# Kernel optimization log

Hardware: AMD Instinct MI355X
Metric: run time of the kernel (lower is better)

## Reference

```python
import jax, jax.numpy as jnp
import numpy as np

BN_EPS = 1e-5


def setup_inputs() -> dict:
    key = jax.random.key(0)
    ks = jax.random.split(key, 8)
    N, Cin, Cout, D, H, W = 4, 512, 256, 256, 128, 128
    feat_ffm = jax.random.normal(ks[0], (N, Cin, H, W), dtype=jnp.float32)
    coarse_x = jax.random.normal(ks[1], (N, D, H, W), dtype=jnp.float32)
    # conv1: 1x1, no bias; BN (eval mode: running stats); conv2: 1x1 with bias
    w1 = jax.random.normal(ks[2], (Cout, Cin), dtype=jnp.float32) * (1.0 / np.sqrt(Cin))
    bn_gamma = jnp.ones((Cout,), dtype=jnp.float32)
    bn_beta = jnp.zeros((Cout,), dtype=jnp.float32)
    bn_mean = jax.random.normal(ks[3], (Cout,), dtype=jnp.float32) * 0.1
    bn_var = jax.random.uniform(ks[4], (Cout,), dtype=jnp.float32, minval=0.5, maxval=1.5)
    w2 = jax.random.normal(ks[5], (Cout, Cout), dtype=jnp.float32) * (1.0 / np.sqrt(Cout))
    b2 = jnp.zeros((Cout,), dtype=jnp.float32)
    return {"feat_ffm": feat_ffm, "coarse_x": coarse_x, "w1": w1,
            "bn_gamma": bn_gamma, "bn_beta": bn_beta, "bn_mean": bn_mean,
            "bn_var": bn_var, "w2": w2, "b2": b2}


def reference(feat_ffm, coarse_x, w1, bn_gamma, bn_beta, bn_mean, bn_var, w2, b2):
    N, D, H, W = coarse_x.shape
    # conv1 (1x1) + BN(eval) + ReLU; Dropout2d is identity in eval mode
    x = jnp.einsum('nihw,oi->nohw', feat_ffm, w1)
    scale = bn_gamma * jax.lax.rsqrt(bn_var + BN_EPS)
    x = x * scale[None, :, None, None] + (bn_beta - bn_mean * scale)[None, :, None, None]
    x = jax.nn.relu(x)  # [N, C, H, W]
    C = x.shape[1]
    q = coarse_x.reshape(N, D, H * W)          # proj_query / proj_value
    k = x.reshape(N, C, H * W)                 # proj_key (pre-permute)
    energy = jnp.einsum('nds,ncs->ndc', q, k)  # [N, D, C]
    energy_new = jnp.max(energy, axis=-1, keepdims=True) - energy
    attention = jax.nn.softmax(energy_new, axis=-1)        # [N, D, C]
    out = jnp.einsum('ndc,nds->ncs', attention, q)         # attention^T @ value
    out = out.reshape(N, C, H, W)
    out = jnp.einsum('nchw,oc->nohw', out, w2) + b2[None, :, None, None]
    return out
```

## Files before the change

kernel.cpp:

```cpp
#include <hip/hip_runtime.h>


#define S_DIM 16384
#define C_DIM 256
#define CIN 512

typedef unsigned short u16;
typedef __attribute__((ext_vector_type(8))) short bf16x8;
typedef __attribute__((ext_vector_type(4))) float f32x4;

__device__ __forceinline__ u16 f2bf(float x) {
    unsigned u = __float_as_uint(x);
    u += 0x7fff + ((u >> 16) & 1);
    return (u16)(u >> 16);
}
__device__ __forceinline__ float bf2f(u16 h) {
    return __uint_as_float(((unsigned)h) << 16);
}
__device__ __forceinline__ void gld16(const u16* g, u16* l) {
    __builtin_amdgcn_global_load_lds((const __attribute__((address_space(1))) void*)g,
                                     (__attribute__((address_space(3))) void*)l, 16, 0, 0);
}
__device__ __forceinline__ void gld16f(const float* g, float* l) {
    __builtin_amdgcn_global_load_lds((const __attribute__((address_space(1))) void*)g,
                                     (__attribute__((address_space(3))) void*)l, 16, 0, 0);
}

__global__ __launch_bounds__(256) void prep_kernel(
    const float* __restrict__ coarse, const float* __restrict__ w1,
    const float* __restrict__ gamma, const float* __restrict__ beta,
    const float* __restrict__ mean, const float* __restrict__ var,
    u16* __restrict__ qhi, u16* __restrict__ qlo,
    u16* __restrict__ w1hi, u16* __restrict__ w1lo, float* __restrict__ b1) {
    int b = blockIdx.x;
    int t = threadIdx.x;
    if (b < 4096) {
        size_t i = (size_t)b * 256 + t;
        for (size_t c = i; c < 4194304u; c += 1048576u) {
            float4 v = ((const float4*)coarse)[c];
            float vv[4] = {v.x, v.y, v.z, v.w};
            u16 h[4], l[4];
#pragma unroll
            for (int j = 0; j < 4; ++j) {
                h[j] = f2bf(vv[j]);
                l[j] = f2bf(vv[j] - bf2f(h[j]));
            }
            *(uint2*)&qhi[c * 4] = *(uint2*)h;
            *(uint2*)&qlo[c * 4] = *(uint2*)l;
        }
    } else {
        int o = (b - 4096) * 16 + (t >> 4);
        int lane16 = t & 15;
        float sc = gamma[o] * rsqrtf(var[o] + 1e-5f);
        for (int i = lane16; i < CIN; i += 16) {
            float v = w1[o * CIN + i] * sc;
            u16 h = f2bf(v);
            w1hi[o * CIN + i] = h;
            w1lo[o * CIN + i] = f2bf(v - bf2f(h));
        }
        if (lane16 == 0) b1[o] = beta[o] - mean[o] * sc;
    }
}

__global__ __launch_bounds__(256) void conv_kernel(
    const u16* __restrict__ w1hi, const u16* __restrict__ w1lo,
    const float* __restrict__ feat, const float* __restrict__ b1,
    u16* __restrict__ khi, u16* __restrict__ klo) {
    __shared__ u16 AhS[4096], AlS[4096];
    __shared__ float BfS[4096];
    int s0 = blockIdx.x * 128;
    int m0 = blockIdx.y * 128;
    int bz = blockIdx.z;
    int tid = threadIdx.x, wave = tid >> 6, lane = tid & 63;
    int quad = lane >> 4, l15 = lane & 15;
    int wm = wave >> 1, wn = wave & 1;

    const u16* gAh0 = w1hi + (size_t)(m0 + lane) * CIN + wave * 8;
    const u16* gAh1 = w1hi + (size_t)(m0 + 64 + lane) * CIN + wave * 8;
    const u16* gAl0 = w1lo + (size_t)(m0 + lane) * CIN + wave * 8;
    const u16* gAl1 = w1lo + (size_t)(m0 + 64 + lane) * CIN + wave * 8;
    u16* dAh = AhS + wave * 1024;
    u16* dAl = AlS + wave * 1024;
    int bcol = ((lane & 31) * 4) ^ ((wave & 1) << 4);
    const float* gB = feat + (size_t)bz * ((size_t)CIN * S_DIM)
                    + (size_t)(8 * wave + (lane >> 5)) * S_DIM + s0 + bcol;
    float* dB = BfS + wave * 1024;

    f32x4 zero = {0.f, 0.f, 0.f, 0.f};
    f32x4 acc[4][4];
#pragma unroll
    for (int i = 0; i < 4; ++i)
#pragma unroll
        for (int j = 0; j < 4; ++j) acc[i][j] = zero;

    for (int kb = 0; kb < CIN; kb += 32) {
        __syncthreads();
        gld16(gAh0 + kb, dAh);
        gld16(gAh1 + kb, dAh + 512);
        gld16(gAl0 + kb, dAl);
        gld16(gAl1 + kb, dAl + 512);
#pragma unroll
        for (int p = 0; p < 4; ++p)
            gld16f(gB + (size_t)(kb + 2 * p) * S_DIM, dB + p * 256);
        __syncthreads();

        bf16x8 a_h[4], a_l[4];
        int aOff = quad * 1024 + (wm * 64 + l15) * 8;
#pragma unroll
        for (int t = 0; t < 4; ++t) {
            a_h[t] = *(const bf16x8*)&AhS[aOff + t * 128];
            a_l[t] = *(const bf16x8*)&AlS[aOff + t * 128];
        }
        bf16x8 b_h[4], b_l[4];
        int fl = (quad & 1) << 4;
        const float* Brow = BfS + quad * 1024;
#pragma unroll
        for (int nt = 0; nt < 4; ++nt) {
            int nf = (wn * 64 + nt * 16 + l15) ^ fl;
            union { unsigned d[4]; bf16x8 v; } H, L;
#pragma unroll
            for (int d = 0; d < 4; ++d) {
                float fa = Brow[(2 * d) * 128 + nf];
                float fb = Brow[(2 * d + 1) * 128 + nf];
                unsigned ua = __float_as_uint(fa), ub = __float_as_uint(fb);
                unsigned ra = ua + 0x7fffu + ((ua >> 16) & 1);
                unsigned rb = ub + 0x7fffu + ((ub >> 16) & 1);
                H.d[d] = __byte_perm(ra, rb, 0x7632);
                unsigned la = __float_as_uint(fa - __uint_as_float(ra & 0xffff0000u));
                unsigned lb = __float_as_uint(fb - __uint_as_float(rb & 0xffff0000u));
                la += 0x7fffu + ((la >> 16) & 1);
                lb += 0x7fffu + ((lb >> 16) & 1);
                L.d[d] = __byte_perm(la, lb, 0x7632);
            }
            b_h[nt] = H.v;
            b_l[nt] = L.v;
        }
#pragma unroll
        for (int mt = 0; mt < 4; ++mt)
#pragma unroll
            for (int nt = 0; nt < 4; ++nt) {
                acc[mt][nt] = __builtin_amdgcn_mfma_f32_16x16x32_bf16(a_h[mt], b_h[nt], acc[mt][nt], 0, 0, 0);
                acc[mt][nt] = __builtin_amdgcn_mfma_f32_16x16x32_bf16(a_h[mt], b_l[nt], acc[mt][nt], 0, 0, 0);
                acc[mt][nt] = __builtin_amdgcn_mfma_f32_16x16x32_bf16(a_l[mt], b_h[nt], acc[mt][nt], 0, 0, 0);
            }
    }

#pragma unroll
    for (int mt = 0; mt < 4; ++mt) {
#pragma unroll
        for (int r = 0; r < 4; ++r) {
            int row = m0 + wm * 64 + mt * 16 + quad * 4 + r;
            float bi = b1[row];
#pragma unroll
            for (int nt = 0; nt < 4; ++nt) {
                int cc = s0 + wn * 64 + nt * 16 + l15;
                float v = fmaxf(acc[mt][nt][r] + bi, 0.f);
                u16 h = f2bf(v);
                size_t o = (size_t)bz * 4194304 + (size_t)row * S_DIM + cc;
                khi[o] = h;
                klo[o] = f2bf(v - bf2f(h));
            }
        }
    }
}

__global__ __launch_bounds__(256) void energy_kernel(
    const u16* __restrict__ qhi, const u16* __restrict__ qlo,
    const u16* __restrict__ khi, const u16* __restrict__ klo,
    float* __restrict__ Ep) {
    __shared__ u16 AhS[4096], BhS[4096], AlS[4096], BlS[4096];
    int kBeg = blockIdx.x * 512;
    int m0 = (blockIdx.y >> 1) * 128;
    int n0 = (blockIdx.y & 1) * 128;
    int bz = blockIdx.z;
    int tid = threadIdx.x, wave = tid >> 6, lane = tid & 63;
    int quad = lane >> 4, l15 = lane & 15;
    int wm = wave >> 1, wn = wave & 1;

    size_t bo = (size_t)bz * 4194304;
    const u16* gAh0 = qhi + bo + (size_t)(m0 + lane) * S_DIM + kBeg + wave * 8;
    const u16* gAh1 = qhi + bo + (size_t)(m0 + 64 + lane) * S_DIM + kBeg + wave * 8;
    const u16* gAl0 = qlo + bo + (size_t)(m0 + lane) * S_DIM + kBeg + wave * 8;
    const u16* gAl1 = qlo + bo + (size_t)(m0 + 64 + lane) * S_DIM + kBeg + wave * 8;
    const u16* gBh0 = khi + bo + (size_t)(n0 + lane) * S_DIM + kBeg + wave * 8;
    const u16* gBh1 = khi + bo + (size_t)(n0 + 64 + lane) * S_DIM + kBeg + wave * 8;
    const u16* gBl0 = klo + bo + (size_t)(n0 + lane) * S_DIM + kBeg + wave * 8;
    const u16* gBl1 = klo + bo + (size_t)(n0 + 64 + lane) * S_DIM + kBeg + wave * 8;
    u16* dAh = AhS + wave * 1024;
    u16* dAl = AlS + wave * 1024;
    u16* dBh = BhS + wave * 1024;
    u16* dBl = BlS + wave * 1024;

    f32x4 zero = {0.f, 0.f, 0.f, 0.f};
    f32x4 acc[4][4];
#pragma unroll
    for (int i = 0; i < 4; ++i)
#pragma unroll
        for (int j = 0; j < 4; ++j) acc[i][j] = zero;

    for (int kb = 0; kb < 512; kb += 32) {
        __syncthreads();
        gld16(gAh0 + kb, dAh);
        gld16(gAh1 + kb, dAh + 512);
        gld16(gBh0 + kb, dBh);
        gld16(gBh1 + kb, dBh + 512);
        gld16(gAl0 + kb, dAl);
        gld16(gAl1 + kb, dAl + 512);
        gld16(gBl0 + kb, dBl);
        gld16(gBl1 + kb, dBl + 512);
        __syncthreads();

        bf16x8 a_h[4], b_h[4], a_l[4], b_l[4];
        int aOff = quad * 1024 + (wm * 64 + l15) * 8;
        int bOff = quad * 1024 + (wn * 64 + l15) * 8;
#pragma unroll
        for (int t = 0; t < 4; ++t) {
            a_h[t] = *(const bf16x8*)&AhS[aOff + t * 128];
            b_h[t] = *(const bf16x8*)&BhS[bOff + t * 128];
            a_l[t] = *(const bf16x8*)&AlS[aOff + t * 128];
            b_l[t] = *(const bf16x8*)&BlS[bOff + t * 128];
        }
#pragma unroll
        for (int mt = 0; mt < 4; ++mt)
#pragma unroll
            for (int nt = 0; nt < 4; ++nt) {
                acc[mt][nt] = __builtin_amdgcn_mfma_f32_16x16x32_bf16(a_h[mt], b_h[nt], acc[mt][nt], 0, 0, 0);
                acc[mt][nt] = __builtin_amdgcn_mfma_f32_16x16x32_bf16(a_h[mt], b_l[nt], acc[mt][nt], 0, 0, 0);
                acc[mt][nt] = __builtin_amdgcn_mfma_f32_16x16x32_bf16(a_l[mt], b_h[nt], acc[mt][nt], 0, 0, 0);
            }
    }

    float* Ce = Ep + ((size_t)(blockIdx.x * 4 + bz)) * 65536;
#pragma unroll
    for (int mt = 0; mt < 4; ++mt)
#pragma unroll
        for (int r = 0; r < 4; ++r) {
            int row = m0 + wm * 64 + mt * 16 + quad * 4 + r;
#pragma unroll
            for (int nt = 0; nt < 4; ++nt) {
                int cc = n0 + wn * 64 + nt * 16 + l15;
                Ce[(size_t)row * C_DIM + cc] = acc[mt][nt][r];
            }
        }
}

__global__ __launch_bounds__(256) void softmax_kernel(const float* __restrict__ Ep,
                                                      float* __restrict__ att) {
    __shared__ float red[4], red2[4];
    int b = blockIdx.x;
    int t = threadIdx.x;
    const float* p = Ep + (size_t)b * 256 + t;
    float v = 0.f;
#pragma unroll 8
    for (int s = 0; s < 32; ++s) v += p[(size_t)s * 262144];
    float m = v;
#pragma unroll
    for (int o = 32; o > 0; o >>= 1) m = fminf(m, __shfl_xor(m, o, 64));
    int lane = t & 63, wid = t >> 6;
    if (lane == 0) red[wid] = m;
    __syncthreads();
    m = fminf(fminf(red[0], red[1]), fminf(red[2], red[3]));
    float e = expf(m - v);
    float s = e;
#pragma unroll
    for (int o = 32; o > 0; o >>= 1) s += __shfl_xor(s, o, 64);
    if (lane == 0) red2[wid] = s;
    __syncthreads();
    s = red2[0] + red2[1] + red2[2] + red2[3];
    att[(size_t)b * 256 + t] = e / s;
}

__global__ __launch_bounds__(256) void m2h_kernel(const float* __restrict__ w2,
                                                  const float* __restrict__ att,
                                                  u16* __restrict__ M2h) {
    int t = blockIdx.x * 256 + threadIdx.x;
    int d = t & 255, o = (t >> 8) & 255, n = t >> 16;
    const float4* wr = (const float4*)(w2 + (size_t)o * C_DIM);
    const float4* ar = (const float4*)(att + ((size_t)n * C_DIM + d) * C_DIM);
    float s = 0.0f;
#pragma unroll 4
    for (int c4 = 0; c4 < 64; ++c4) {
        float4 w = wr[c4];
        float4 a = ar[c4];
        s += w.x * a.x + w.y * a.y + w.z * a.z + w.w * a.w;
    }
    M2h[((size_t)n * C_DIM + o) * C_DIM + d] = f2bf(s);
}

__global__ __launch_bounds__(256) void final_kernel(
    const u16* __restrict__ M2h, const float* __restrict__ coarse,
    const float* __restrict__ b2, float* __restrict__ out) {
    __shared__ u16 AhS[4096];
    __shared__ float BfS[4096];
    int s0 = blockIdx.x * 128;
    int m0 = blockIdx.y * 128;
    int bz = blockIdx.z;
    int tid = threadIdx.x, wave = tid >> 6, lane = tid & 63;
    int quad = lane >> 4, l15 = lane & 15;
    int wm = wave >> 1, wn = wave & 1;

    const u16* gA0 = M2h + (size_t)bz * 65536 + (size_t)(m0 + lane) * C_DIM + wave * 8;
    const u16* gA1 = M2h + (size_t)bz * 65536 + (size_t)(m0 + 64 + lane) * C_DIM + wave * 8;
    u16* dA = AhS + wave * 1024;
    int bcol = ((lane & 31) * 4) ^ ((wave & 1) << 4);
    const float* gB = coarse + (size_t)bz * 4194304
                    + (size_t)(8 * wave + (lane >> 5)) * S_DIM + s0 + bcol;
    float* dB = BfS + wave * 1024;

    f32x4 zero = {0.f, 0.f, 0.f, 0.f};
    f32x4 acc[4][4];
#pragma unroll
    for (int i = 0; i < 4; ++i)
#pragma unroll
        for (int j = 0; j < 4; ++j) acc[i][j] = zero;

    for (int kb = 0; kb < C_DIM; kb += 32) {
        __syncthreads();
        gld16(gA0 + kb, dA);
        gld16(gA1 + kb, dA + 512);
#pragma unroll
        for (int p = 0; p < 4; ++p)
            gld16f(gB + (size_t)(kb + 2 * p) * S_DIM, dB + p * 256);
        __syncthreads();

        bf16x8 a_h[4];
        int aOff = quad * 1024 + (wm * 64 + l15) * 8;
#pragma unroll
        for (int t = 0; t < 4; ++t) a_h[t] = *(const bf16x8*)&AhS[aOff + t * 128];
        bf16x8 b_h[4];
        int fl = (quad & 1) << 4;
        const float* Brow = BfS + quad * 1024;
#pragma unroll
        for (int nt = 0; nt < 4; ++nt) {
            int nf = (wn * 64 + nt * 16 + l15) ^ fl;
            union { unsigned d[4]; bf16x8 v; } H;
#pragma unroll
            for (int d = 0; d < 4; ++d) {
                float fa = Brow[(2 * d) * 128 + nf];
                float fb = Brow[(2 * d + 1) * 128 + nf];
                unsigned ua = __float_as_uint(fa), ub = __float_as_uint(fb);
                unsigned ra = ua + 0x7fffu + ((ua >> 16) & 1);
                unsigned rb = ub + 0x7fffu + ((ub >> 16) & 1);
                H.d[d] = __byte_perm(ra, rb, 0x7632);
            }
            b_h[nt] = H.v;
        }
#pragma unroll
        for (int mt = 0; mt < 4; ++mt)
#pragma unroll
            for (int nt = 0; nt < 4; ++nt)
                acc[mt][nt] = __builtin_amdgcn_mfma_f32_16x16x32_bf16(a_h[mt], b_h[nt], acc[mt][nt], 0, 0, 0);
    }

#pragma unroll
    for (int mt = 0; mt < 4; ++mt)
#pragma unroll
        for (int r = 0; r < 4; ++r) {
            int row = m0 + wm * 64 + mt * 16 + quad * 4 + r;
            float bi = b2[row];
#pragma unroll
            for (int nt = 0; nt < 4; ++nt) {
                int cc = s0 + wn * 64 + nt * 16 + l15;
                out[(size_t)bz * 4194304 + (size_t)row * S_DIM + cc] = acc[mt][nt][r] + bi;
            }
        }
}

extern "C" void kernel_launch(void* const* d_in, const int* in_sizes, int n_in,
                              void* d_out, int out_size, void* d_ws, size_t ws_size,
                              hipStream_t stream) {
    const float* feat   = (const float*)d_in[0];
    const float* coarse = (const float*)d_in[1];
    const float* w1     = (const float*)d_in[2];
    const float* gamma  = (const float*)d_in[3];
    const float* beta   = (const float*)d_in[4];
    const float* mean   = (const float*)d_in[5];
    const float* var    = (const float*)d_in[6];
    const float* w2     = (const float*)d_in[7];
    const float* b2     = (const float*)d_in[8];
    float* out = (float*)d_out;

    char* base = (char*)d_ws;
    u16* qhi   = (u16*)(base);
    u16* qlo   = (u16*)(base + 33554432);
    u16* khi   = (u16*)(base + 67108864);
    u16* klo   = (u16*)(base + 100663296);
    float* Ep  = (float*)(base + 134217728);
    float* att = (float*)(base + 201326592);
    u16* M2h   = (u16*)(base + 202375168);
    u16* w1hi  = (u16*)(base + 202899456);
    u16* w1lo  = (u16*)(base + 203161600);
    float* b1  = (float*)(base + 203423744);

    prep_kernel<<<4112, 256, 0, stream>>>(coarse, w1, gamma, beta, mean, var,
                                          qhi, qlo, w1hi, w1lo, b1);

    conv_kernel<<<dim3(128, 2, 4), 256, 0, stream>>>(w1hi, w1lo, feat, b1, khi, klo);

    energy_kernel<<<dim3(32, 4, 4), 256, 0, stream>>>(qhi, qlo, khi, klo, Ep);

    softmax_kernel<<<1024, 256, 0, stream>>>(Ep, att);

    m2h_kernel<<<1024, 256, 0, stream>>>(w2, att, M2h);

    final_kernel<<<dim3(128, 2, 4), 256, 0, stream>>>(M2h, coarse, b2, out);
}
```

Baseline: 460.4 us.

## Switch split-precision GEMMs from bf16 to fp16 and swizzle LDS tile layout

Replaces the bf16 hi/lo split with fp16 hi/lo across all GEMM stages, using fp16 MFMA. In the conv and final kernels the fp32 B operand is now rounded straight to a single fp16 value, which cuts the conv from three MFMAs to two per tile and removes the lo-part conversion arithmetic. LDS A/B tiles are reorganised row-major with an XOR swizzle on the k-chunk to reduce bank conflicts on fragment reads. fp16's narrower exponent range risks overflow or underflow on the activations and on the energy inputs.

```diff
diff --git a/kernel.cpp b/kernel.cpp
--- a/kernel.cpp
+++ b/kernel.cpp
@@ -6,16 +6,17 @@
 #define CIN 512
 
 typedef unsigned short u16;
-typedef __attribute__((ext_vector_type(8))) short bf16x8;
+typedef _Float16 f16;
+typedef __attribute__((ext_vector_type(8))) _Float16 f16x8;
 typedef __attribute__((ext_vector_type(4))) float f32x4;
 
-__device__ __forceinline__ u16 f2bf(float x) {
-    unsigned u = __float_as_uint(x);
-    u += 0x7fff + ((u >> 16) & 1);
-    return (u16)(u >> 16);
-}
-__device__ __forceinline__ float bf2f(u16 h) {
-    return __uint_as_float(((unsigned)h) << 16);
+__device__ __forceinline__ u16 f2h(float x) {
+    f16 h = (f16)x;
+    return *(u16*)&h;
+}
+__device__ __forceinline__ float h2f(u16 u) {
+    f16 h = *(f16*)&u;
+    return (float)h;
 }
 __device__ __forceinline__ void gld16(const u16* g, u16* l) {
     __builtin_amdgcn_global_load_lds((const __attribute__((address_space(1))) void*)g,
@@ -42,8 +43,8 @@
             u16 h[4], l[4];
 #pragma unroll
             for (int j = 0; j < 4; ++j) {
-                h[j] = f2bf(vv[j]);
-                l[j] = f2bf(vv[j] - bf2f(h[j]));
+                h[j] = f2h(vv[j]);
+                l[j] = f2h(vv[j] - h2f(h[j]));
             }
             *(uint2*)&qhi[c * 4] = *(uint2*)h;
             *(uint2*)&qlo[c * 4] = *(uint2*)l;
@@ -54,9 +55,9 @@
         float sc = gamma[o] * rsqrtf(var[o] + 1e-5f);
         for (int i = lane16; i < CIN; i += 16) {
             float v = w1[o * CIN + i] * sc;
-            u16 h = f2bf(v);
+            u16 h = f2h(v);
             w1hi[o * CIN + i] = h;
-            w1lo[o * CIN + i] = f2bf(v - bf2f(h));
+            w1lo[o * CIN + i] = f2h(v - h2f(h));
         }
         if (lane16 == 0) b1[o] = beta[o] - mean[o] * sc;
     }
@@ -75,12 +76,13 @@
     int quad = lane >> 4, l15 = lane & 15;
     int wm = wave >> 1, wn = wave & 1;
 
-    const u16* gAh0 = w1hi + (size_t)(m0 + lane) * CIN + wave * 8;
-    const u16* gAh1 = w1hi + (size_t)(m0 + 64 + lane) * CIN + wave * 8;
-    const u16* gAl0 = w1lo + (size_t)(m0 + lane) * CIN + wave * 8;
-    const u16* gAl1 = w1lo + (size_t)(m0 + 64 + lane) * CIN + wave * 8;
+    int Lr = lane >> 2, Ls = lane & 3;
+    int koff = (Ls ^ ((Lr >> 1) & 3)) * 8;
+    const u16* gAh = w1hi + (size_t)(m0 + wave * 32 + Lr) * CIN + koff;
+    const u16* gAl = w1lo + (size_t)(m0 + wave * 32 + Lr) * CIN + koff;
     u16* dAh = AhS + wave * 1024;
     u16* dAl = AlS + wave * 1024;
+
     int bcol = ((lane & 31) * 4) ^ ((wave & 1) << 4);
     const float* gB = feat + (size_t)bz * ((size_t)CIN * S_DIM)
                     + (size_t)(8 * wave + (lane >> 5)) * S_DIM + s0 + bcol;
@@ -95,53 +97,40 @@
 
     for (int kb = 0; kb < CIN; kb += 32) {
         __syncthreads();
-        gld16(gAh0 + kb, dAh);
-        gld16(gAh1 + kb, dAh + 512);
-        gld16(gAl0 + kb, dAl);
-        gld16(gAl1 + kb, dAl + 512);
+        gld16(gAh + kb, dAh);
+        gld16(gAh + kb + 16 * CIN, dAh + 512);
+        gld16(gAl + kb, dAl);
+        gld16(gAl + kb + 16 * CIN, dAl + 512);
 #pragma unroll
         for (int p = 0; p < 4; ++p)
             gld16f(gB + (size_t)(kb + 2 * p) * S_DIM, dB + p * 256);
         __syncthreads();
 
-        bf16x8 a_h[4], a_l[4];
-        int aOff = quad * 1024 + (wm * 64 + l15) * 8;
+        f16x8 a_h[4], a_l[4];
+        int axor = ((l15 >> 1) & 3);
+        int ao = (wm * 64 + l15) * 32 + ((quad ^ axor) * 8);
 #pragma unroll
         for (int t = 0; t < 4; ++t) {
-            a_h[t] = *(const bf16x8*)&AhS[aOff + t * 128];
-            a_l[t] = *(const bf16x8*)&AlS[aOff + t * 128];
-        }
-        bf16x8 b_h[4], b_l[4];
+            a_h[t] = *(const f16x8*)&AhS[ao + t * 512];
+            a_l[t] = *(const f16x8*)&AlS[ao + t * 512];
+        }
+        f16x8 b_s[4];
         int fl = (quad & 1) << 4;
         const float* Brow = BfS + quad * 1024;
 #pragma unroll
         for (int nt = 0; nt < 4; ++nt) {
             int nf = (wn * 64 + nt * 16 + l15) ^ fl;
-            union { unsigned d[4]; bf16x8 v; } H, L;
-#pragma unroll
-            for (int d = 0; d < 4; ++d) {
-                float fa = Brow[(2 * d) * 128 + nf];
-                float fb = Brow[(2 * d + 1) * 128 + nf];
-                unsigned ua = __float_as_uint(fa), ub = __float_as_uint(fb);
-                unsigned ra = ua + 0x7fffu + ((ua >> 16) & 1);
-                unsigned rb = ub + 0x7fffu + ((ub >> 16) & 1);
-                H.d[d] = __byte_perm(ra, rb, 0x7632);
-                unsigned la = __float_as_uint(fa - __uint_as_float(ra & 0xffff0000u));
-                unsigned lb = __float_as_uint(fb - __uint_as_float(rb & 0xffff0000u));
-                la += 0x7fffu + ((la >> 16) & 1);
-                lb += 0x7fffu + ((lb >> 16) & 1);
-                L.d[d] = __byte_perm(la, lb, 0x7632);
-            }
-            b_h[nt] = H.v;
-            b_l[nt] = L.v;
+            union { u16 u[8]; f16x8 v; } T;
+#pragma unroll
+            for (int j = 0; j < 8; ++j) T.u[j] = f2h(Brow[j * 128 + nf]);
+            b_s[nt] = T.v;
         }
 #pragma unroll
         for (int mt = 0; mt < 4; ++mt)
 #pragma unroll
             for (int nt = 0; nt < 4; ++nt) {
-                acc[mt][nt] = __builtin_amdgcn_mfma_f32_16x16x32_bf16(a_h[mt], b_h[nt], acc[mt][nt], 0, 0, 0);
-                acc[mt][nt] = __builtin_amdgcn_mfma_f32_16x16x32_bf16(a_h[mt], b_l[nt], acc[mt][nt], 0, 0, 0);
-                acc[mt][nt] = __builtin_amdgcn_mfma_f32_16x16x32_bf16(a_l[mt], b_h[nt], acc[mt][nt], 0, 0, 0);
+                acc[mt][nt] = __builtin_amdgcn_mfma_f32_16x16x32_f16(a_h[mt], b_s[nt], acc[mt][nt], 0, 0, 0);
+                acc[mt][nt] = __builtin_amdgcn_mfma_f32_16x16x32_f16(a_l[mt], b_s[nt], acc[mt][nt], 0, 0, 0);
             }
     }
 
@@ -155,10 +144,10 @@
             for (int nt = 0; nt < 4; ++nt) {
                 int cc = s0 + wn * 64 + nt * 16 + l15;
                 float v = fmaxf(acc[mt][nt][r] + bi, 0.f);
-                u16 h = f2bf(v);
+                u16 h = f2h(v);
                 size_t o = (size_t)bz * 4194304 + (size_t)row * S_DIM + cc;
                 khi[o] = h;
-                klo[o] = f2bf(v - bf2f(h));
+                klo[o] = f2h(v - h2f(h));
             }
         }
     }
@@ -177,15 +166,13 @@
     int quad = lane >> 4, l15 = lane & 15;
     int wm = wave >> 1, wn = wave & 1;
 
+    int Lr = lane >> 2, Ls = lane & 3;
+    int koff = (Ls ^ ((Lr >> 1) & 3)) * 8;
     size_t bo = (size_t)bz * 4194304;
-    const u16* gAh0 = qhi + bo + (size_t)(m0 + lane) * S_DIM + kBeg + wave * 8;
-    const u16* gAh1 = qhi + bo + (size_t)(m0 + 64 + lane) * S_DIM + kBeg + wave * 8;
-    const u16* gAl0 = qlo + bo + (size_t)(m0 + lane) * S_DIM + kBeg + wave * 8;
-    const u16* gAl1 = qlo + bo + (size_t)(m0 + 64 + lane) * S_DIM + kBeg + wave * 8;
-    const u16* gBh0 = khi + bo + (size_t)(n0 + lane) * S_DIM + kBeg + wave * 8;
-    const u16* gBh1 = khi + bo + (size_t)(n0 + 64 + lane) * S_DIM + kBeg + wave * 8;
-    const u16* gBl0 = klo + bo + (size_t)(n0 + lane) * S_DIM + kBeg + wave * 8;
-    const u16* gBl1 = klo + bo + (size_t)(n0 + 64 + lane) * S_DIM + kBeg + wave * 8;
+    const u16* gAh = qhi + bo + (size_t)(m0 + wave * 32 + Lr) * S_DIM + kBeg + koff;
+    const u16* gAl = qlo + bo + (size_t)(m0 + wave * 32 + Lr) * S_DIM + kBeg + koff;
+    const u16* gBh = khi + bo + (size_t)(n0 + wave * 32 + Lr) * S_DIM + kBeg + koff;
+    const u16* gBl = klo + bo + (size_t)(n0 + wave * 32 + Lr) * S_DIM + kBeg + koff;
     u16* dAh = AhS + wave * 1024;
     u16* dAl = AlS + wave * 1024;
     u16* dBh = BhS + wave * 1024;
@@ -198,35 +185,37 @@
 #pragma unroll
         for (int j = 0; j < 4; ++j) acc[i][j] = zero;
 
+    const size_t row16 = (size_t)16 * S_DIM;
     for (int kb = 0; kb < 512; kb += 32) {
         __syncthreads();
-        gld16(gAh0 + kb, dAh);
-        gld16(gAh1 + kb, dAh + 512);
-        gld16(gBh0 + kb, dBh);
-        gld16(gBh1 + kb, dBh + 512);
-        gld16(gAl0 + kb, dAl);
-        gld16(gAl1 + kb, dAl + 512);
-        gld16(gBl0 + kb, dBl);
-        gld16(gBl1 + kb, dBl + 512);
-        __syncthreads();
-
-        bf16x8 a_h[4], b_h[4], a_l[4], b_l[4];
-        int aOff = quad * 1024 + (wm * 64 + l15) * 8;
-        int bOff = quad * 1024 + (wn * 64 + l15) * 8;
+        gld16(gAh + kb, dAh);
+        gld16(gAh + kb + row16, dAh + 512);
+        gld16(gBh + kb, dBh);
+        gld16(gBh + kb + row16, dBh + 512);
+        gld16(gAl + kb, dAl);
+        gld16(gAl + kb + row16, dAl + 512);
+        gld16(gBl + kb, dBl);
+        gld16(gBl + kb + row16, dBl + 512);
+        __syncthreads();
+
+        f16x8 a_h[4], b_h[4], a_l[4], b_l[4];
+        int axor = ((l15 >> 1) & 3);
+        int aOff = (wm * 64 + l15) * 32 + ((quad ^ axor) * 8);
+        int bOff = (wn * 64 + l15) * 32 + ((quad ^ axor) * 8);
 #pragma unroll
         for (int t = 0; t < 4; ++t) {
-            a_h[t] = *(const bf16x8*)&AhS[aOff + t * 128];
-            b_h[t] = *(const bf16x8*)&BhS[bOff + t * 128];
-            a_l[t] = *(const bf16x8*)&AlS[aOff + t * 128];
-            b_l[t] = *(const bf16x8*)&BlS[bOff + t * 128];
+            a_h[t] = *(const f16x8*)&AhS[aOff + t * 512];
+            b_h[t] = *(const f16x8*)&BhS[bOff + t * 512];
+            a_l[t] = *(const f16x8*)&AlS[aOff + t * 512];
+            b_l[t] = *(const f16x8*)&BlS[bOff + t * 512];
         }
 #pragma unroll
         for (int mt = 0; mt < 4; ++mt)
 #pragma unroll
             for (int nt = 0; nt < 4; ++nt) {
-                acc[mt][nt] = __builtin_amdgcn_mfma_f32_16x16x32_bf16(a_h[mt], b_h[nt], acc[mt][nt], 0, 0, 0);
-                acc[mt][nt] = __builtin_amdgcn_mfma_f32_16x16x32_bf16(a_h[mt], b_l[nt], acc[mt][nt], 0, 0, 0);
-                acc[mt][nt] = __builtin_amdgcn_mfma_f32_16x16x32_bf16(a_l[mt], b_h[nt], acc[mt][nt], 0, 0, 0);
+                acc[mt][nt] = __builtin_amdgcn_mfma_f32_16x16x32_f16(a_h[mt], b_h[nt], acc[mt][nt], 0, 0, 0);
+                acc[mt][nt] = __builtin_amdgcn_mfma_f32_16x16x32_f16(a_h[mt], b_l[nt], acc[mt][nt], 0, 0, 0);
+                acc[mt][nt] = __builtin_amdgcn_mfma_f32_16x16x32_f16(a_l[mt], b_h[nt], acc[mt][nt], 0, 0, 0);
             }
     }
 
@@ -284,7 +273,7 @@
         float4 a = ar[c4];
         s += w.x * a.x + w.y * a.y + w.z * a.z + w.w * a.w;
     }
-    M2h[((size_t)n * C_DIM + o) * C_DIM + d] = f2bf(s);
+    M2h[((size_t)n * C_DIM + o) * C_DIM + d] = f2h(s);
 }
 
 __global__ __launch_bounds__(256) void final_kernel(
@@ -299,8 +288,9 @@
     int quad = lane >> 4, l15 = lane & 15;
     int wm = wave >> 1, wn = wave & 1;
 
-    const u16* gA0 = M2h + (size_t)bz * 65536 + (size_t)(m0 + lane) * C_DIM + wave * 8;
-    const u16* gA1 = M2h + (size_t)bz * 65536 + (size_t)(m0 + 64 + lane) * C_DIM + wave * 8;
+    int Lr = lane >> 2, Ls = lane & 3;
+    int koff = (Ls ^ ((Lr >> 1) & 3)) * 8;
+    const u16* gA = M2h + (size_t)bz * 65536 + (size_t)(m0 + wave * 32 + Lr) * C_DIM + koff;
     u16* dA = AhS + wave * 1024;
     int bcol = ((lane & 31) * 4) ^ ((wave & 1) << 4);
     const float* gB = coarse + (size_t)bz * 4194304
@@ -316,40 +306,34 @@
 
     for (int kb = 0; kb < C_DIM; kb += 32) {
         __syncthreads();
-        gld16(gA0 + kb, dA);
-        gld16(gA1 + kb, dA + 512);
+        gld16(gA + kb, dA);
+        gld16(gA + kb + 16 * C_DIM, dA + 512);
 #pragma unroll
         for (int p = 0; p < 4; ++p)
             gld16f(gB + (size_t)(kb + 2 * p) * S_DIM, dB + p * 256);
         __syncthreads();
 
-        bf16x8 a_h[4];
-        int aOff = quad * 1024 + (wm * 64 + l15) * 8;
-#pragma unroll
-        for (int t = 0; t < 4; ++t) a_h[t] = *(const bf16x8*)&AhS[aOff + t * 128];
-        bf16x8 b_h[4];
+        f16x8 a_s[4];
+        int axor = ((l15 >> 1) & 3);
+        int ao = (wm * 64 + l15) * 32 + ((quad ^ axor) * 8);
+#pragma unroll
+        for (int t = 0; t < 4; ++t) a_s[t] = *(const f16x8*)&AhS[ao + t * 512];
+        f16x8 b_s[4];
         int fl = (quad & 1) << 4;
         const float* Brow = BfS + quad * 1024;
 #pragma unroll
         for (int nt = 0; nt < 4; ++nt) {
             int nf = (wn * 64 + nt * 16 + l15) ^ fl;
-            union { unsigned d[4]; bf16x8 v; } H;
-#pragma unroll
-            for (int d = 0; d < 4; ++d) {
-                float fa = Brow[(2 * d) * 128 + nf];
-                float fb = Brow[(2 * d + 1) * 128 + nf];
-                unsigned ua = __float_as_uint(fa), ub = __float_as_uint(fb);
-                unsigned ra = ua + 0x7fffu + ((ua >> 16) & 1);
-                unsigned rb = ub + 0x7fffu + ((ub >> 16) & 1);
-                H.d[d] = __byte_perm(ra, rb, 0x7632);
-            }
-            b_h[nt] = H.v;
+            union { u16 u[8]; f16x8 v; } T;
+#pragma unroll
+            for (int j = 0; j < 8; ++j) T.u[j] = f2h(Brow[j * 128 + nf]);
+            b_s[nt] = T.v;
         }
 #pragma unroll
         for (int mt = 0; mt < 4; ++mt)
 #pragma unroll
             for (int nt = 0; nt < 4; ++nt)
-                acc[mt][nt] = __builtin_amdgcn_mfma_f32_16x16x32_bf16(a_h[mt], b_h[nt], acc[mt][nt], 0, 0, 0);
+                acc[mt][nt] = __builtin_amdgcn_mfma_f32_16x16x32_f16(a_s[mt], b_s[nt], acc[mt][nt], 0, 0, 0);
     }
 
 #pragma unroll
```

Measured after the change: 428.6 us. 1.07x faster.
